# Optimization experiments

Measured on AMD Instinct MI355X. Metric: run time of the kernel, lower is better.

## Reference

```python
import jax, jax.numpy as jnp
import numpy as np

H = 32          # num attention heads
KVH = 8         # num kv heads
D = 64          # head dim
HID = 2048      # hidden size
MAXB = 1024     # max_bias_length
BASE = 10000.0  # rope theta


def _rope(x, pos):
    # x: (B, S, h, D), pos: (S,) -- GPT-NeoX half-split rotary
    half = D // 2
    inv_freq = 1.0 / (BASE ** (jnp.arange(0, D, 2, dtype=jnp.float32) / D))  # (half,)
    ang = pos[:, None].astype(jnp.float32) * inv_freq                         # (S, half)
    cos = jnp.cos(ang)[None, :, None, :]
    sin = jnp.sin(ang)[None, :, None, :]
    x1, x2 = x[..., :half], x[..., half:]
    return jnp.concatenate([x1 * cos - x2 * sin, x2 * cos + x1 * sin], axis=-1)


def setup_inputs() -> dict:
    key = jax.random.key(0)
    ks = jax.random.split(key, 7)
    B, S = 2, 1024
    hidden_states = jax.random.normal(ks[0], (B, S, HID), dtype=jnp.float32)
    attention_mask = jnp.broadcast_to(
        jnp.tril(jnp.ones((S, S), dtype=jnp.int32))[None, None], (B, 1, S, S))
    # weights stored as (in, out): y = x @ W  (same math as torch Linear)
    Wq = jax.random.normal(ks[1], (HID, H * D), dtype=jnp.float32) * 0.02
    Wk = jax.random.normal(ks[2], (HID, KVH * D), dtype=jnp.float32) * 0.02
    Wv = jax.random.normal(ks[3], (HID, KVH * D), dtype=jnp.float32) * 0.02
    Wo = jax.random.normal(ks[4], (H * D, HID), dtype=jnp.float32) * 0.02
    bias_diag = jax.random.normal(ks[5], (H, MAXB), dtype=jnp.float32) * 0.001
    softmax_offset = jnp.zeros((H,), dtype=jnp.float32)
    return {"hidden_states": hidden_states, "attention_mask": attention_mask,
            "Wq": Wq, "Wk": Wk, "Wv": Wv, "Wo": Wo,
            "bias_diag": bias_diag, "softmax_offset": softmax_offset}


def reference(hidden_states, attention_mask, Wq, Wk, Wv, Wo, bias_diag, softmax_offset):
    B, S, _ = hidden_states.shape
    scaling = D ** (-0.5)
    pos = jnp.arange(S)

    q = (hidden_states @ Wq).reshape(B, S, H, D)
    k = (hidden_states @ Wk).reshape(B, S, KVH, D)
    v = (hidden_states @ Wv).reshape(B, S, KVH, D)

    q = _rope(q, pos)
    k = _rope(k, pos)

    # (B, H, S, D); repeat_kv via repeat on head axis
    q = q.transpose(0, 2, 1, 3)
    k = jnp.repeat(k.transpose(0, 2, 1, 3), H // KVH, axis=1)
    v = jnp.repeat(v.transpose(0, 2, 1, 3), H // KVH, axis=1)

    scores = jnp.einsum('bhqd,bhkd->bhqk', q, k) * scaling

    # learnable diagonal relative-position bias
    rel = pos[:, None] - pos[None, :]                     # (S, S)
    valid = ((rel >= 0) & (rel < MAXB)).astype(scores.dtype)
    idx = jnp.clip(rel, 0, MAXB - 1)
    bias = bias_diag[:, idx] * valid                      # (H, S, S)
    scores = scores + bias[None]

    scores = jnp.where(attention_mask[:, :, :, :S] == 0, -jnp.inf, scores)

    weights = jax.nn.softmax(scores.astype(jnp.float32), axis=-1)

    # adaptive offset subtraction + relu
    offset = jnp.abs(softmax_offset + 1.0)[None, :, None, None]
    num_visible = (pos + 1).astype(jnp.float32)[None, None, :, None]  # along query dim
    weights = jax.nn.relu(weights - offset / num_visible)

    attn_out = jnp.einsum('bhqk,bhkd->bhqd', weights.astype(v.dtype), v)
    attn_out = attn_out.transpose(0, 2, 1, 3).reshape(B, S, H * D)
    return attn_out @ Wo
```

## Files before the change

kernel.cpp:

```cpp
#include <hip/hip_runtime.h>
#include <cstdint>
#include <cstddef>

#define BB   2
#define SS   1024
#define HID  2048
#define HH   32
#define KVHH 8
#define DD   64
#define NQKV 3072
#define QKW  2560

typedef __attribute__((ext_vector_type(8))) short bf16x8;
typedef __attribute__((ext_vector_type(4))) float f32x4;
typedef __attribute__((ext_vector_type(4))) unsigned int u32x4;

__device__ __forceinline__ unsigned short f2bf(float f) {
    unsigned int u = __float_as_uint(f);
    unsigned int r = (u + 0x7fffu + ((u >> 16) & 1u)) >> 16;
    return (unsigned short)r;
}

__device__ __forceinline__ void g2l16(const unsigned short* g, unsigned short* l) {
    __builtin_amdgcn_global_load_lds(
        (__attribute__((address_space(1))) void*)(unsigned short*)g,
        (__attribute__((address_space(3))) void*)l,
        16, 0, 0);
}

__global__ __launch_bounds__(256) void prep(
    const float* __restrict__ hidden,
    const float* __restrict__ Wq, const float* __restrict__ Wk,
    const float* __restrict__ Wv, const float* __restrict__ Wo,
    unsigned short* __restrict__ hidden_bf,
    unsigned short* __restrict__ WqkvT,
    unsigned short* __restrict__ WoT)
{
    const int z   = blockIdx.z;
    const int tid = threadIdx.x;

    if (z == 4) {
        int r0 = blockIdx.y * 64, c0 = blockIdx.x * 64;
        #pragma unroll
        for (int p = 0; p < 4; ++p) {
            int f = tid + p * 256;
            int row = r0 + (f >> 4), c4 = c0 + (f & 15) * 4;
            float4 v = *(const float4*)&hidden[(size_t)row * 2048 + c4];
            ushort4 o;
            o.x = f2bf(v.x); o.y = f2bf(v.y); o.z = f2bf(v.z); o.w = f2bf(v.w);
            *(ushort4*)&hidden_bf[(size_t)row * 2048 + c4] = o;
        }
        return;
    }

    const float* W;
    unsigned short* Wt;
    int N;
    if (z == 0)      { W = Wq; Wt = WqkvT;                        N = 2048; }
    else if (z == 1) { W = Wk; Wt = WqkvT + (size_t)2048 * 2048;  N = 512;  }
    else if (z == 2) { W = Wv; Wt = WqkvT + (size_t)2560 * 2048;  N = 512;  }
    else             { W = Wo; Wt = WoT;                          N = 2048; }
    if (blockIdx.x * 64 >= N) return;

    __shared__ float t[64][68];
    const int n0 = blockIdx.x * 64, k0 = blockIdx.y * 64;
    #pragma unroll
    for (int p = 0; p < 4; ++p) {
        int f = tid + p * 256;
        int row = f >> 4, c4 = (f & 15) * 4;
        float4 v = *(const float4*)&W[(size_t)(k0 + row) * N + n0 + c4];
        t[row][c4 + 0] = v.x; t[row][c4 + 1] = v.y;
        t[row][c4 + 2] = v.z; t[row][c4 + 3] = v.w;
    }
    __syncthreads();
    #pragma unroll
    for (int p = 0; p < 4; ++p) {
        int f = tid + p * 256;
        int nrow = f >> 4, kc4 = (f & 15) * 4;
        ushort4 o;
        o.x = f2bf(t[kc4 + 0][nrow]);
        o.y = f2bf(t[kc4 + 1][nrow]);
        o.z = f2bf(t[kc4 + 2][nrow]);
        o.w = f2bf(t[kc4 + 3][nrow]);
        *(ushort4*)&Wt[(size_t)(n0 + nrow) * 2048 + k0 + kc4] = o;
    }
}

__global__ __launch_bounds__(256) void gemm_qkv_fused(
    const unsigned short* __restrict__ A,
    const unsigned short* __restrict__ Bt,
    unsigned short* __restrict__ qk_bf,
    unsigned short* __restrict__ v_t)
{
    __shared__ __align__(16) char smem[33024];
    short* Asb = (short*)smem;
    short* Bsb = (short*)(smem + 16384);
    float* Ctf = (float*)smem;

    const int tid  = threadIdx.x;
    const int lane = tid & 63;
    const int wave = tid >> 6;
    const int quad = lane >> 4;
    const int l15  = lane & 15;
    const int wm = (wave >> 1) * 64, wn = (wave & 1) * 64;
    const int m0 = blockIdx.y * 128, n0 = blockIdx.x * 128;
    const int K = 2048;

    f32x4 acc[4][4] = {};

    for (int k0 = 0; k0 < K; k0 += 64) {
        #pragma unroll
        for (int p = 0; p < 4; ++p) {
            int ci = tid + p * 256;
            int row = ci >> 3, sc = (ci & 7) ^ (row & 7);
            g2l16(&A[(size_t)(m0 + row) * K + k0 + sc * 8],
                  (unsigned short*)Asb + ci * 8);
        }
        #pragma unroll
        for (int p = 0; p < 4; ++p) {
            int ci = tid + p * 256;
            int row = ci >> 3, sc = (ci & 7) ^ (row & 7);
            g2l16(&Bt[(size_t)(n0 + row) * K + k0 + sc * 8],
                  (unsigned short*)Bsb + ci * 8);
        }
        __syncthreads();

        #pragma unroll
        for (int s = 0; s < 2; ++s) {
            bf16x8 af[4], bfr[4];
            #pragma unroll
            for (int i = 0; i < 4; ++i) {
                int row = wm + i * 16 + l15;
                af[i] = *(const bf16x8*)(Asb + row * 64 +
                        ((((s << 2) | quad) ^ (row & 7)) * 8));
            }
            #pragma unroll
            for (int j = 0; j < 4; ++j) {
                int row = wn + j * 16 + l15;
                bfr[j] = *(const bf16x8*)(Bsb + row * 64 +
                        ((((s << 2) | quad) ^ (row & 7)) * 8));
            }
            #pragma unroll
            for (int i = 0; i < 4; ++i)
                #pragma unroll
                for (int j = 0; j < 4; ++j)
                    acc[i][j] = __builtin_amdgcn_mfma_f32_16x16x32_bf16(
                        af[i], bfr[j], acc[i][j], 0, 0, 0);
        }
        __syncthreads();
    }

    const int bx = blockIdx.x;
    const int b  = m0 >> 10;
    const int s0 = m0 & 1023;
    const int hcg = bx * 128;

    #pragma unroll 1
    for (int ph = 0; ph < 2; ++ph) {
        if (ph) __syncthreads();
        if ((wave >> 1) == ph) {
            #pragma unroll
            for (int i = 0; i < 4; ++i)
                #pragma unroll
                for (int j = 0; j < 4; ++j)
                    #pragma unroll
                    for (int rg = 0; rg < 4; ++rg)
                        Ctf[(i * 16 + quad * 4 + rg) * 129 + wn + j * 16 + l15]
                            = acc[i][j][rg];
        }
        __syncthreads();

        if (bx < 20) {
            const float scale = (bx < 16) ? 0.125f : 1.0f;
            #pragma unroll
            for (int p = 0; p < 4; ++p) {
                int idx = tid + p * 256;
                int row = idx >> 4, hi = (idx >> 3) & 1, t0 = (idx & 7) * 4;
                int s = s0 + ph * 64 + row;
                ushort4 o1, o2;
                #pragma unroll
                for (int k = 0; k < 4; ++k) {
                    int t = t0 + k;
                    float x1 = Ctf[row * 129 + hi * 64 + t];
                    float x2 = Ctf[row * 129 + hi * 64 + t + 32];
                    float inv = __expf(-(float)t * 0.28782313662425572f);
                    float ang = (float)s * inv;
                    float c  = __cosf(ang);
                    float sn = __sinf(ang);
                    ((unsigned short*)&o1)[k] = f2bf((x1 * c - x2 * sn) * scale);
                    ((unsigned short*)&o2)[k] = f2bf((x2 * c + x1 * sn) * scale);
                }
                unsigned short* dst =
                    qk_bf + (size_t)(m0 + ph * 64 + row) * QKW + hcg + hi * 64;
                *(ushort4*)&dst[t0]      = o1;
                *(ushort4*)&dst[t0 + 32] = o2;
            }
        } else {
            const int vb = b * 512 + (bx - 20) * 128;
            #pragma unroll
            for (int p = 0; p < 8; ++p) {
                int idx = tid + p * 256;
                int cc = idx >> 4, srow = (idx & 15) * 4;
                ushort4 o;
                #pragma unroll
                for (int k = 0; k < 4; ++k)
                    ((unsigned short*)&o)[k] = f2bf(Ctf[(srow + k) * 129 + cc]);
                *(ushort4*)&v_t[(size_t)(vb + cc) * 1024 + s0 + ph * 64 + srow] = o;
            }
        }
    }
}

__global__ __launch_bounds__(256) void gemm_bf16_bt(
    const unsigned short* __restrict__ A,
    const unsigned short* __restrict__ Bt,
    float* __restrict__ C, int M, int N, int K)
{
    __shared__ short Asb[128 * 64];
    __shared__ short Bsb[64 * 64];

    const int tid  = threadIdx.x;
    const int lane = tid & 63;
    const int wave = tid >> 6;
    const int quad = lane >> 4;
    const int l15  = lane & 15;
    const int wm = (wave >> 1) * 64, wn = (wave & 1) * 32;
    const int m0 = blockIdx.y * 128, n0 = blockIdx.x * 64;

    f32x4 acc[4][2] = {};

    for (int k0 = 0; k0 < K; k0 += 64) {
        #pragma unroll
        for (int p = 0; p < 4; ++p) {
            int ci = tid + p * 256;
            int row = ci >> 3, sc = (ci & 7) ^ (row & 7);
            g2l16(&A[(size_t)(m0 + row) * K + k0 + sc * 8],
                  (unsigned short*)Asb + ci * 8);
        }
        #pragma unroll
        for (int p = 0; p < 2; ++p) {
            int ci = tid + p * 256;
            int row = ci >> 3, sc = (ci & 7) ^ (row & 7);
            g2l16(&Bt[(size_t)(n0 + row) * K + k0 + sc * 8],
                  (unsigned short*)Bsb + ci * 8);
        }
        __syncthreads();

        #pragma unroll
        for (int s = 0; s < 2; ++s) {
            bf16x8 af[4], bfr[2];
            #pragma unroll
            for (int i = 0; i < 4; ++i) {
                int row = wm + i * 16 + l15;
                af[i] = *(const bf16x8*)(Asb + row * 64 +
                        ((((s << 2) | quad) ^ (row & 7)) * 8));
            }
            #pragma unroll
            for (int j = 0; j < 2; ++j) {
                int row = wn + j * 16 + l15;
                bfr[j] = *(const bf16x8*)(Bsb + row * 64 +
                        ((((s << 2) | quad) ^ (row & 7)) * 8));
            }
            #pragma unroll
            for (int i = 0; i < 4; ++i)
                #pragma unroll
                for (int j = 0; j < 2; ++j)
                    acc[i][j] = __builtin_amdgcn_mfma_f32_16x16x32_bf16(
                        af[i], bfr[j], acc[i][j], 0, 0, 0);
        }
        __syncthreads();
    }

    #pragma unroll
    for (int i = 0; i < 4; ++i) {
        int grow = m0 + wm + i * 16 + quad * 4;
        #pragma unroll
        for (int j = 0; j < 2; ++j) {
            int gcol = n0 + wn + j * 16 + l15;
            #pragma unroll
            for (int rg = 0; rg < 4; ++rg)
                C[(size_t)(grow + rg) * N + gcol] = acc[i][j][rg];
        }
    }
}

__global__ __launch_bounds__(256, 4) void attn_mfma(
    const unsigned short* __restrict__ qk_bf,
    const unsigned short* __restrict__ v_t,
    const float* __restrict__ bias_diag,
    const float* __restrict__ soff,
    unsigned short* __restrict__ AO)
{
    static const unsigned char qtab[16] =
        {15, 14, 13, 12, 10, 11, 8, 9, 4, 5, 6, 7, 1, 0, 3, 2};
    const int id = (int)blockIdx.x;
    const int qt = qtab[(id >> 6) & 15];
    const int h  = id & 31;
    const int b  = (id >> 5) & 1;
    const int kh = h >> 2;
    const int tid  = threadIdx.x;
    const int lane = tid & 63;
    const int wave = tid >> 6;
    const int quad = lane >> 4;
    const int l15  = lane & 15;
    const int q0   = qt * 64;

    __shared__ short Ks[2][4096];
    __shared__ short Vs[2][4096];
    __shared__ float bd_s[1024];

    for (int i = tid; i < 1024; i += 256) bd_s[i] = bias_diag[h * 1024 + i];

    const unsigned short* Qg = qk_bf + (size_t)(b * SS + q0 + wave * 16) * QKW + h * 64;
    const unsigned short* Kg = qk_bf + (size_t)(b * SS) * QKW + 2048 + kh * 64;
    const unsigned short* Vg = v_t + (size_t)(b * 512 + kh * 64) * SS;

    const int qrow = q0 + wave * 16 + l15;

    bf16x8 qf0 = *(const bf16x8*)(Qg + (size_t)l15 * QKW + quad * 8);
    bf16x8 qf1 = *(const bf16x8*)(Qg + (size_t)l15 * QKW + 32 + quad * 8);

#define STAGE_K(j, buf) do {                                                  \
    _Pragma("unroll")                                                         \
    for (int p = 0; p < 2; ++p) {                                             \
        int ci = tid + p * 256;                                               \
        int row_ = ci >> 3;                                                   \
        int sc_  = (ci & 7) ^ (row_ & 7);                                     \
        g2l16(Kg + (size_t)((j) * 64 + row_) * QKW + sc_ * 8,                 \
              (unsigned short*)&Ks[buf][ci * 8]);                             \
    } } while (0)

#define STAGE_V(j, buf) do {                                                  \
    _Pragma("unroll")                                                         \
    for (int p = 0; p < 2; ++p) {                                             \
        int ci = tid + p * 256;                                               \
        int row_ = ci >> 3;                                                   \
        int sc_  = (ci & 7) ^ (row_ & 7);                                     \
        g2l16(Vg + (size_t)row_ * SS + (j) * 64 + sc_ * 8,                    \
              (unsigned short*)&Vs[buf][ci * 8]);                             \
    } } while (0)

    float lpa[4] = {0.f, 0.f, 0.f, 0.f};
    STAGE_K(0, 0);
    __syncthreads();
    int cur = 0;
    for (int j = 0; j <= qt; ++j) {
        if (j < qt) STAGE_K(j + 1, cur ^ 1);
        const short* Kb = Ks[cur];
        const bool diag = (j == qt);

        f32x4 acc[4] = {};
        #pragma unroll
        for (int nb = 0; nb < 4; ++nb) {
            if (diag && nb > wave) continue;
            int row = nb * 16 + l15, sw = row & 7;
            bf16x8 a0 = *(const bf16x8*)(Kb + row * 64 + ((quad ^ sw) * 8));
            bf16x8 a1 = *(const bf16x8*)(Kb + row * 64 + (((quad + 4) ^ sw) * 8));
            acc[nb] = __builtin_amdgcn_mfma_f32_16x16x32_bf16(a0, qf0, acc[nb], 0, 0, 0);
            acc[nb] = __builtin_amdgcn_mfma_f32_16x16x32_bf16(a1, qf1, acc[nb], 0, 0, 0);
        }
        if (!diag) {
            #pragma unroll
            for (int nb = 0; nb < 4; ++nb) {
                int rel0 = qrow - (j * 64 + nb * 16 + quad * 4);
                #pragma unroll
                for (int r = 0; r < 4; ++r)
                    lpa[r] += __expf(acc[nb][r] + bd_s[rel0 - r]);
            }
        } else {
            #pragma unroll
            for (int nb = 0; nb < 4; ++nb) {
                if (nb > wave) continue;
                #pragma unroll
                for (int r = 0; r < 4; ++r) {
                    int rel = qrow - (j * 64 + nb * 16 + quad * 4 + r);
                    if (rel >= 0) lpa[r] += __expf(acc[nb][r] + bd_s[rel]);
                }
            }
        }
        __syncthreads();
        cur ^= 1;
    }

    float lp = (lpa[0] + lpa[1]) + (lpa[2] + lpa[3]);
    lp += __shfl_xor(lp, 16, 64);
    lp += __shfl_xor(lp, 32, 64);
    const float invl = 1.f / lp;
    const float cl   = fabsf(soff[h] + 1.f) / (float)(qrow + 1) * lp;

    f32x4 oacc[4] = {};
    STAGE_K(0, 0);
    STAGE_V(0, 0);
    __syncthreads();
    cur = 0;
    for (int j = 0; j <= qt; ++j) {
        if (j < qt) { STAGE_K(j + 1, cur ^ 1); STAGE_V(j + 1, cur ^ 1); }
        const short* Kb = Ks[cur];
        const short* Vb = Vs[cur];
        const bool diag = (j == qt);

        f32x4 acc[4] = {};
        #pragma unroll
        for (int nb = 0; nb < 4; ++nb) {
            if (diag && nb > wave) continue;
            int row = nb * 16 + l15, sw = row & 7;
            bf16x8 a0 = *(const bf16x8*)(Kb + row * 64 + ((quad ^ sw) * 8));
            bf16x8 a1 = *(const bf16x8*)(Kb + row * 64 + (((quad + 4) ^ sw) * 8));
            acc[nb] = __builtin_amdgcn_mfma_f32_16x16x32_bf16(a0, qf0, acc[nb], 0, 0, 0);
            acc[nb] = __builtin_amdgcn_mfma_f32_16x16x32_bf16(a1, qf1, acc[nb], 0, 0, 0);
        }

        unsigned int pk[4][2];
        #pragma unroll
        for (int nb = 0; nb < 4; ++nb) {
            float w[4];
            #pragma unroll
            for (int r = 0; r < 4; ++r) {
                int rel = qrow - (j * 64 + nb * 16 + quad * 4 + r);
                float e = 0.f;
                if (rel >= 0)
                    e = fmaxf(__expf(acc[nb][r] + bd_s[rel]) - cl, 0.f);
                w[r] = e;
            }
            asm("v_cvt_pk_bf16_f32 %0, %1, %2" : "=v"(pk[nb][0]) : "v"(w[0]), "v"(w[1]));
            asm("v_cvt_pk_bf16_f32 %0, %1, %2" : "=v"(pk[nb][1]) : "v"(w[2]), "v"(w[3]));
        }
        unsigned int ppk[4][2];
        #pragma unroll
        for (int nb = 0; nb < 4; ++nb) {
            ppk[nb][0] = __shfl_xor(pk[nb][0], 16, 64);
            ppk[nb][1] = __shfl_xor(pk[nb][1], 16, 64);
        }

        const bool oddq = quad & 1;
        const int  cv   = ((quad & 1) << 1) | (quad >> 1);
        #pragma unroll
        for (int s = 0; s < 2; ++s) {
            if (diag && s == 1 && wave < 2) continue;
            unsigned int w0 = oddq ? ppk[2 * s + 1][0] : pk[2 * s][0];
            unsigned int w1 = oddq ? ppk[2 * s + 1][1] : pk[2 * s][1];
            unsigned int w2 = oddq ? pk[2 * s + 1][0]  : ppk[2 * s][0];
            unsigned int w3 = oddq ? pk[2 * s + 1][1]  : ppk[2 * s][1];
            u32x4 t; t[0] = w0; t[1] = w1; t[2] = w2; t[3] = w3;
            bf16x8 pf = __builtin_bit_cast(bf16x8, t);
            #pragma unroll
            for (int nd = 0; nd < 4; ++nd) {
                int rowv = nd * 16 + l15, swv = rowv & 7;
                bf16x8 vf = *(const bf16x8*)(Vb + rowv * 64 + (((cv + 4 * s) ^ swv) * 8));
                oacc[nd] = __builtin_amdgcn_mfma_f32_16x16x32_bf16(pf, vf, oacc[nd], 0, 0, 0);
            }
        }
        __syncthreads();
        cur ^= 1;
    }

    float invl_r[4];
    #pragma unroll
    for (int r = 0; r < 4; ++r)
        invl_r[r] = __shfl(invl, quad * 4 + r, 64);

    unsigned short* aop = AO + (size_t)(b * SS + q0 + wave * 16 + quad * 4) * 2048
                             + h * 64 + l15;
    #pragma unroll
    for (int nd = 0; nd < 4; ++nd)
        #pragma unroll
        for (int r = 0; r < 4; ++r)
            aop[(size_t)r * 2048 + nd * 16] = f2bf(oacc[nd][r] * invl_r[r]);
#undef STAGE_K
#undef STAGE_V
}

extern "C" void kernel_launch(void* const* d_in, const int* in_sizes, int n_in,
                              void* d_out, int out_size, void* d_ws, size_t ws_size,
                              hipStream_t stream)
{
    const float* hidden    = (const float*)d_in[0];
    const float* Wq        = (const float*)d_in[2];
    const float* Wk        = (const float*)d_in[3];
    const float* Wv        = (const float*)d_in[4];
    const float* Wo        = (const float*)d_in[5];
    const float* bias_diag = (const float*)d_in[6];
    const float* soff      = (const float*)d_in[7];
    float* out = (float*)d_out;

    char* wsb = (char*)d_ws;
    unsigned short* hidden_bf = (unsigned short*)wsb;
    unsigned short* WqkvT     = (unsigned short*)(wsb + (size_t)8388608);
    unsigned short* AO_bf     = (unsigned short*)(wsb + (size_t)12582912);
    unsigned short* WoT       = (unsigned short*)(wsb + (size_t)20971520);
    unsigned short* qk_bf     = (unsigned short*)(wsb + (size_t)29360128);
    unsigned short* v_t       = (unsigned short*)(wsb + (size_t)29360128 + (size_t)2048 * 2560 * 2);

    prep<<<dim3(32, 32, 5), dim3(256), 0, stream>>>(
        hidden, Wq, Wk, Wv, Wo, hidden_bf, WqkvT, WoT);

    gemm_qkv_fused<<<dim3(24, 16), dim3(256), 0, stream>>>(
        hidden_bf, WqkvT, qk_bf, v_t);

    attn_mfma<<<dim3(1024), dim3(256), 0, stream>>>(
        qk_bf, v_t, bias_diag, soff, AO_bf);

    gemm_bf16_bt<<<dim3(2048 / 64, 2048 / 128), dim3(256), 0, stream>>>(
        AO_bf, WoT, out, 2048, 2048, 2048);
}
```

Measured before the change: 230.0 us.

## Split KV tiles across two wave groups and pair causal query tiles per block

The attention kernel now launches 512 blocks of 512 threads. Each block handles two query tiles, qt and 15-qt, so work across blocks is balanced under the causal mask. Within a block, two groups of four waves take alternating KV tiles, and their row sums and output accumulators are combined through shared memory. This is meant to cut causal load imbalance and shorten the serial KV loop per query tile, at the cost of extra shared-memory reductions, more barriers and higher LDS use per block.

```diff
diff --git a/kernel.cpp b/kernel.cpp
--- a/kernel.cpp
+++ b/kernel.cpp
@@ -284,188 +284,234 @@
     }
 }
 
-__global__ __launch_bounds__(256, 4) void attn_mfma(
+__global__ __launch_bounds__(512, 4) void attn_mfma(
     const unsigned short* __restrict__ qk_bf,
     const unsigned short* __restrict__ v_t,
     const float* __restrict__ bias_diag,
     const float* __restrict__ soff,
     unsigned short* __restrict__ AO)
 {
-    static const unsigned char qtab[16] =
-        {15, 14, 13, 12, 10, 11, 8, 9, 4, 5, 6, 7, 1, 0, 3, 2};
     const int id = (int)blockIdx.x;
-    const int qt = qtab[(id >> 6) & 15];
     const int h  = id & 31;
     const int b  = (id >> 5) & 1;
+    const int pi = id >> 6;
     const int kh = h >> 2;
     const int tid  = threadIdx.x;
     const int lane = tid & 63;
     const int wave = tid >> 6;
+    const int grp  = wave >> 2;
+    const int w4   = wave & 3;
+    const int gt   = tid & 255;
     const int quad = lane >> 4;
     const int l15  = lane & 15;
-    const int q0   = qt * 64;
-
-    __shared__ short Ks[2][4096];
-    __shared__ short Vs[2][4096];
+
+    __shared__ short Ks[2][2][4096];
+    __shared__ short Vs[2][2][4096];
     __shared__ float bd_s[1024];
-
-    for (int i = tid; i < 1024; i += 256) bd_s[i] = bias_diag[h * 1024 + i];
-
-    const unsigned short* Qg = qk_bf + (size_t)(b * SS + q0 + wave * 16) * QKW + h * 64;
+    __shared__ float red[2][64];
+
+    for (int i = tid; i < 1024; i += 512) bd_s[i] = bias_diag[h * 1024 + i];
+
     const unsigned short* Kg = qk_bf + (size_t)(b * SS) * QKW + 2048 + kh * 64;
     const unsigned short* Vg = v_t + (size_t)(b * 512 + kh * 64) * SS;
 
-    const int qrow = q0 + wave * 16 + l15;
-
-    bf16x8 qf0 = *(const bf16x8*)(Qg + (size_t)l15 * QKW + quad * 8);
-    bf16x8 qf1 = *(const bf16x8*)(Qg + (size_t)l15 * QKW + 32 + quad * 8);
+    short* KsG = &Ks[grp][0][0];
+    short* VsG = &Vs[grp][0][0];
+    float* Fred = (float*)&Ks[1][0][0];
 
 #define STAGE_K(j, buf) do {                                                  \
     _Pragma("unroll")                                                         \
     for (int p = 0; p < 2; ++p) {                                             \
-        int ci = tid + p * 256;                                               \
+        int ci = gt + p * 256;                                                \
         int row_ = ci >> 3;                                                   \
         int sc_  = (ci & 7) ^ (row_ & 7);                                     \
         g2l16(Kg + (size_t)((j) * 64 + row_) * QKW + sc_ * 8,                 \
-              (unsigned short*)&Ks[buf][ci * 8]);                             \
+              (unsigned short*)(KsG + (buf) * 4096 + ci * 8));                \
     } } while (0)
 
 #define STAGE_V(j, buf) do {                                                  \
     _Pragma("unroll")                                                         \
     for (int p = 0; p < 2; ++p) {                                             \
-        int ci = tid + p * 256;                                               \
+        int ci = gt + p * 256;                                                \
         int row_ = ci >> 3;                                                   \
         int sc_  = (ci & 7) ^ (row_ & 7);                                     \
         g2l16(Vg + (size_t)row_ * SS + (j) * 64 + sc_ * 8,                    \
-              (unsigned short*)&Vs[buf][ci * 8]);                             \
+              (unsigned short*)(VsG + (buf) * 4096 + ci * 8));                \
     } } while (0)
 
-    float lpa[4] = {0.f, 0.f, 0.f, 0.f};
-    STAGE_K(0, 0);
-    __syncthreads();
-    int cur = 0;
-    for (int j = 0; j <= qt; ++j) {
-        if (j < qt) STAGE_K(j + 1, cur ^ 1);
-        const short* Kb = Ks[cur];
-        const bool diag = (j == qt);
-
-        f32x4 acc[4] = {};
-        #pragma unroll
-        for (int nb = 0; nb < 4; ++nb) {
-            if (diag && nb > wave) continue;
-            int row = nb * 16 + l15, sw = row & 7;
-            bf16x8 a0 = *(const bf16x8*)(Kb + row * 64 + ((quad ^ sw) * 8));
-            bf16x8 a1 = *(const bf16x8*)(Kb + row * 64 + (((quad + 4) ^ sw) * 8));
-            acc[nb] = __builtin_amdgcn_mfma_f32_16x16x32_bf16(a0, qf0, acc[nb], 0, 0, 0);
-            acc[nb] = __builtin_amdgcn_mfma_f32_16x16x32_bf16(a1, qf1, acc[nb], 0, 0, 0);
-        }
-        if (!diag) {
-            #pragma unroll
-            for (int nb = 0; nb < 4; ++nb) {
-                int rel0 = qrow - (j * 64 + nb * 16 + quad * 4);
+    #pragma unroll 1
+    for (int half = 0; half < 2; ++half) {
+        const int qt = half ? pi : 15 - pi;
+        const int q0 = qt * 64;
+        const int nI = (qt + 2) >> 1;
+        const int qrow = q0 + w4 * 16 + l15;
+
+        const unsigned short* Qg =
+            qk_bf + (size_t)(b * SS + q0 + w4 * 16) * QKW + h * 64;
+        bf16x8 qf0 = *(const bf16x8*)(Qg + (size_t)l15 * QKW + quad * 8);
+        bf16x8 qf1 = *(const bf16x8*)(Qg + (size_t)l15 * QKW + 32 + quad * 8);
+
+        float lpa[4] = {0.f, 0.f, 0.f, 0.f};
+        if (grp <= qt) STAGE_K(grp, 0);
+        __syncthreads();
+        int cur = 0;
+        for (int i = 0; i < nI; ++i) {
+            const int j = 2 * i + grp;
+            if (j + 2 <= qt) STAGE_K(j + 2, cur ^ 1);
+            if (j <= qt) {
+                const short* Kb = KsG + cur * 4096;
+                const bool diag = (j == qt);
+                f32x4 acc[4] = {};
+                #pragma unroll
+                for (int nb = 0; nb < 4; ++nb) {
+                    if (diag && nb > w4) continue;
+                    int row = nb * 16 + l15, sw = row & 7;
+                    bf16x8 a0 = *(const bf16x8*)(Kb + row * 64 + ((quad ^ sw) * 8));
+                    bf16x8 a1 = *(const bf16x8*)(Kb + row * 64 + (((quad + 4) ^ sw) * 8));
+                    acc[nb] = __builtin_amdgcn_mfma_f32_16x16x32_bf16(a0, qf0, acc[nb], 0, 0, 0);
+                    acc[nb] = __builtin_amdgcn_mfma_f32_16x16x32_bf16(a1, qf1, acc[nb], 0, 0, 0);
+                }
+                if (!diag) {
+                    #pragma unroll
+                    for (int nb = 0; nb < 4; ++nb) {
+                        int rel0 = qrow - (j * 64 + nb * 16 + quad * 4);
+                        #pragma unroll
+                        for (int r = 0; r < 4; ++r)
+                            lpa[r] += __expf(acc[nb][r] + bd_s[rel0 - r]);
+                    }
+                } else {
+                    #pragma unroll
+                    for (int nb = 0; nb < 4; ++nb) {
+                        if (nb > w4) continue;
+                        #pragma unroll
+                        for (int r = 0; r < 4; ++r) {
+                            int rel = qrow - (j * 64 + nb * 16 + quad * 4 + r);
+                            if (rel >= 0) lpa[r] += __expf(acc[nb][r] + bd_s[rel]);
+                        }
+                    }
+                }
+            }
+            __syncthreads();
+            cur ^= 1;
+        }
+
+        float lp = (lpa[0] + lpa[1]) + (lpa[2] + lpa[3]);
+        lp += __shfl_xor(lp, 16, 64);
+        lp += __shfl_xor(lp, 32, 64);
+        if (quad == 0) red[grp][w4 * 16 + l15] = lp;
+        __syncthreads();
+        lp = red[0][w4 * 16 + l15] + red[1][w4 * 16 + l15];
+        const float invl = 1.f / lp;
+        const float cl   = fabsf(soff[h] + 1.f) / (float)(qrow + 1) * lp;
+
+        f32x4 oacc[4] = {};
+        if (grp <= qt) { STAGE_K(grp, 0); STAGE_V(grp, 0); }
+        __syncthreads();
+        cur = 0;
+        for (int i = 0; i < nI; ++i) {
+            const int j = 2 * i + grp;
+            if (j + 2 <= qt) { STAGE_K(j + 2, cur ^ 1); STAGE_V(j + 2, cur ^ 1); }
+            if (j <= qt) {
+                const short* Kb = KsG + cur * 4096;
+                const short* Vb = VsG + cur * 4096;
+                const bool diag = (j == qt);
+
+                f32x4 acc[4] = {};
+                #pragma unroll
+                for (int nb = 0; nb < 4; ++nb) {
+                    if (diag && nb > w4) continue;
+                    int row = nb * 16 + l15, sw = row & 7;
+                    bf16x8 a0 = *(const bf16x8*)(Kb + row * 64 + ((quad ^ sw) * 8));
+                    bf16x8 a1 = *(const bf16x8*)(Kb + row * 64 + (((quad + 4) ^ sw) * 8));
+                    acc[nb] = __builtin_amdgcn_mfma_f32_16x16x32_bf16(a0, qf0, acc[nb], 0, 0, 0);
+                    acc[nb] = __builtin_amdgcn_mfma_f32_16x16x32_bf16(a1, qf1, acc[nb], 0, 0, 0);
+                }
+
+                unsigned int pk[4][2];
+                if (!diag) {
+                    #pragma unroll
+                    for (int nb = 0; nb < 4; ++nb) {
+                        float w[4];
+                        int rel0 = qrow - (j * 64 + nb * 16 + quad * 4);
+                        #pragma unroll
+                        for (int r = 0; r < 4; ++r)
+                            w[r] = fmaxf(__expf(acc[nb][r] + bd_s[rel0 - r]) - cl, 0.f);
+                        asm("v_cvt_pk_bf16_f32 %0, %1, %2" : "=v"(pk[nb][0]) : "v"(w[0]), "v"(w[1]));
+                        asm("v_cvt_pk_bf16_f32 %0, %1, %2" : "=v"(pk[nb][1]) : "v"(w[2]), "v"(w[3]));
+                    }
+                } else {
+                    #pragma unroll
+                    for (int nb = 0; nb < 4; ++nb) {
+                        float w[4];
+                        #pragma unroll
+                        for (int r = 0; r < 4; ++r) {
+                            int rel = qrow - (j * 64 + nb * 16 + quad * 4 + r);
+                            float e = 0.f;
+                            if (rel >= 0)
+                                e = fmaxf(__expf(acc[nb][r] + bd_s[rel]) - cl, 0.f);
+                            w[r] = e;
+                        }
+                        asm("v_cvt_pk_bf16_f32 %0, %1, %2" : "=v"(pk[nb][0]) : "v"(w[0]), "v"(w[1]));
+                        asm("v_cvt_pk_bf16_f32 %0, %1, %2" : "=v"(pk[nb][1]) : "v"(w[2]), "v"(w[3]));
+                    }
+                }
+                unsigned int ppk[4][2];
+                #pragma unroll
+                for (int nb = 0; nb < 4; ++nb) {
+                    ppk[nb][0] = __shfl_xor(pk[nb][0], 16, 64);
+                    ppk[nb][1] = __shfl_xor(pk[nb][1], 16, 64);
+                }
+
+                const bool oddq = quad & 1;
+                const int  cv   = ((quad & 1) << 1) | (quad >> 1);
+                #pragma unroll
+                for (int s = 0; s < 2; ++s) {
+                    if (diag && s == 1 && w4 < 2) continue;
+                    unsigned int w0 = oddq ? ppk[2 * s + 1][0] : pk[2 * s][0];
+                    unsigned int w1 = oddq ? ppk[2 * s + 1][1] : pk[2 * s][1];
+                    unsigned int w2 = oddq ? pk[2 * s + 1][0]  : ppk[2 * s][0];
+                    unsigned int w3 = oddq ? pk[2 * s + 1][1]  : ppk[2 * s][1];
+                    u32x4 t; t[0] = w0; t[1] = w1; t[2] = w2; t[3] = w3;
+                    bf16x8 pf = __builtin_bit_cast(bf16x8, t);
+                    #pragma unroll
+                    for (int nd = 0; nd < 4; ++nd) {
+                        int rowv = nd * 16 + l15, swv = rowv & 7;
+                        bf16x8 vf = *(const bf16x8*)(Vb + rowv * 64 + (((cv + 4 * s) ^ swv) * 8));
+                        oacc[nd] = __builtin_amdgcn_mfma_f32_16x16x32_bf16(pf, vf, oacc[nd], 0, 0, 0);
+                    }
+                }
+            }
+            __syncthreads();
+            cur ^= 1;
+        }
+
+        if (grp == 1) {
+            #pragma unroll
+            for (int nd = 0; nd < 4; ++nd)
                 #pragma unroll
                 for (int r = 0; r < 4; ++r)
-                    lpa[r] += __expf(acc[nb][r] + bd_s[rel0 - r]);
-            }
-        } else {
-            #pragma unroll
-            for (int nb = 0; nb < 4; ++nb) {
-                if (nb > wave) continue;
+                    Fred[(w4 * 16 + quad * 4 + r) * 64 + nd * 16 + l15] = oacc[nd][r];
+        }
+        __syncthreads();
+        if (grp == 0) {
+            float invl_r[4];
+            #pragma unroll
+            for (int r = 0; r < 4; ++r)
+                invl_r[r] = __shfl(invl, quad * 4 + r, 64);
+            unsigned short* aop =
+                AO + (size_t)(b * SS + q0 + w4 * 16 + quad * 4) * 2048 + h * 64 + l15;
+            #pragma unroll
+            for (int nd = 0; nd < 4; ++nd)
                 #pragma unroll
                 for (int r = 0; r < 4; ++r) {
-                    int rel = qrow - (j * 64 + nb * 16 + quad * 4 + r);
-                    if (rel >= 0) lpa[r] += __expf(acc[nb][r] + bd_s[rel]);
-                }
-            }
-        }
-        __syncthreads();
-        cur ^= 1;
-    }
-
-    float lp = (lpa[0] + lpa[1]) + (lpa[2] + lpa[3]);
-    lp += __shfl_xor(lp, 16, 64);
-    lp += __shfl_xor(lp, 32, 64);
-    const float invl = 1.f / lp;
-    const float cl   = fabsf(soff[h] + 1.f) / (float)(qrow + 1) * lp;
-
-    f32x4 oacc[4] = {};
-    STAGE_K(0, 0);
-    STAGE_V(0, 0);
-    __syncthreads();
-    cur = 0;
-    for (int j = 0; j <= qt; ++j) {
-        if (j < qt) { STAGE_K(j + 1, cur ^ 1); STAGE_V(j + 1, cur ^ 1); }
-        const short* Kb = Ks[cur];
-        const short* Vb = Vs[cur];
-        const bool diag = (j == qt);
-
-        f32x4 acc[4] = {};
-        #pragma unroll
-        for (int nb = 0; nb < 4; ++nb) {
-            if (diag && nb > wave) continue;
-            int row = nb * 16 + l15, sw = row & 7;
-            bf16x8 a0 = *(const bf16x8*)(Kb + row * 64 + ((quad ^ sw) * 8));
-            bf16x8 a1 = *(const bf16x8*)(Kb + row * 64 + (((quad + 4) ^ sw) * 8));
-            acc[nb] = __builtin_amdgcn_mfma_f32_16x16x32_bf16(a0, qf0, acc[nb], 0, 0, 0);
-            acc[nb] = __builtin_amdgcn_mfma_f32_16x16x32_bf16(a1, qf1, acc[nb], 0, 0, 0);
-        }
-
-        unsigned int pk[4][2];
-        #pragma unroll
-        for (int nb = 0; nb < 4; ++nb) {
-            float w[4];
-            #pragma unroll
-            for (int r = 0; r < 4; ++r) {
-                int rel = qrow - (j * 64 + nb * 16 + quad * 4 + r);
-                float e = 0.f;
-                if (rel >= 0)
-                    e = fmaxf(__expf(acc[nb][r] + bd_s[rel]) - cl, 0.f);
-                w[r] = e;
-            }
-            asm("v_cvt_pk_bf16_f32 %0, %1, %2" : "=v"(pk[nb][0]) : "v"(w[0]), "v"(w[1]));
-            asm("v_cvt_pk_bf16_f32 %0, %1, %2" : "=v"(pk[nb][1]) : "v"(w[2]), "v"(w[3]));
-        }
-        unsigned int ppk[4][2];
-        #pragma unroll
-        for (int nb = 0; nb < 4; ++nb) {
-            ppk[nb][0] = __shfl_xor(pk[nb][0], 16, 64);
-            ppk[nb][1] = __shfl_xor(pk[nb][1], 16, 64);
-        }
-
-        const bool oddq = quad & 1;
-        const int  cv   = ((quad & 1) << 1) | (quad >> 1);
-        #pragma unroll
-        for (int s = 0; s < 2; ++s) {
-            if (diag && s == 1 && wave < 2) continue;
-            unsigned int w0 = oddq ? ppk[2 * s + 1][0] : pk[2 * s][0];
-            unsigned int w1 = oddq ? ppk[2 * s + 1][1] : pk[2 * s][1];
-            unsigned int w2 = oddq ? pk[2 * s + 1][0]  : ppk[2 * s][0];
-            unsigned int w3 = oddq ? pk[2 * s + 1][1]  : ppk[2 * s][1];
-            u32x4 t; t[0] = w0; t[1] = w1; t[2] = w2; t[3] = w3;
-            bf16x8 pf = __builtin_bit_cast(bf16x8, t);
-            #pragma unroll
-            for (int nd = 0; nd < 4; ++nd) {
-                int rowv = nd * 16 + l15, swv = rowv & 7;
-                bf16x8 vf = *(const bf16x8*)(Vb + rowv * 64 + (((cv + 4 * s) ^ swv) * 8));
-                oacc[nd] = __builtin_amdgcn_mfma_f32_16x16x32_bf16(pf, vf, oacc[nd], 0, 0, 0);
-            }
-        }
-        __syncthreads();
-        cur ^= 1;
-    }
-
-    float invl_r[4];
-    #pragma unroll
-    for (int r = 0; r < 4; ++r)
-        invl_r[r] = __shfl(invl, quad * 4 + r, 64);
-
-    unsigned short* aop = AO + (size_t)(b * SS + q0 + wave * 16 + quad * 4) * 2048
-                             + h * 64 + l15;
-    #pragma unroll
-    for (int nd = 0; nd < 4; ++nd)
-        #pragma unroll
-        for (int r = 0; r < 4; ++r)
-            aop[(size_t)r * 2048 + nd * 16] = f2bf(oacc[nd][r] * invl_r[r]);
+                    float o = (oacc[nd][r] +
+                               Fred[(w4 * 16 + quad * 4 + r) * 64 + nd * 16 + l15])
+                              * invl_r[r];
+                    aop[(size_t)r * 2048 + nd * 16] = f2bf(o);
+                }
+        }
+        __syncthreads();
+    }
 #undef STAGE_K
 #undef STAGE_V
 }
@@ -497,7 +543,7 @@
     gemm_qkv_fused<<<dim3(24, 16), dim3(256), 0, stream>>>(
         hidden_bf, WqkvT, qk_bf, v_t);
 
-    attn_mfma<<<dim3(1024), dim3(256), 0, stream>>>(
+    attn_mfma<<<dim3(512), dim3(512), 0, stream>>>(
         qk_bf, v_t, bias_diag, soff, AO_bf);
 
     gemm_bf16_bt<<<dim3(2048 / 64, 2048 / 128), dim3(256), 0, stream>>>(
```

New measurement: 226.1 us. Within noise of the previous version (-1.7%).
